# Optimization experiments

Measured on AMD Instinct MI355X. Metric: run time of the kernel, lower is better.

The kernel has to match this reference:

```python
import jax, jax.numpy as jnp
import numpy as np

N, E, F_IN, HID, HEADS = 10000, 160000, 70, 256, 4
NEG_SLOPE = 0.2


def setup_inputs() -> dict:
    key = jax.random.key(0)
    ks = jax.random.split(key, 12)
    p = lambda k, shape: jax.random.normal(k, shape, jnp.float32) * 0.05
    return dict(
        node_features=jax.random.normal(ks[0], (N, F_IN), jnp.float32),
        edge_index=jax.random.randint(ks[1], (2, E), 0, N),
        edge_attr=jax.random.normal(ks[2], (E, 4), jnp.float32),
        W1=p(ks[3], (F_IN, HEADS * HID)),
        att_src1=p(ks[4], (HEADS, HID)),
        att_dst1=p(ks[5], (HEADS, HID)),
        b1=jnp.zeros((HEADS * HID,), jnp.float32),
        W2=p(ks[6], (HEADS * HID, HID)),
        att_src2=p(ks[7], (1, HID)),
        att_dst2=p(ks[8], (1, HID)),
        b2=jnp.zeros((HID,), jnp.float32),
        Wv1=p(ks[9], (HID, 128)),
        bv1=jnp.zeros((128,), jnp.float32),
        Wv2=p(ks[10], (128, 1)),
        bv2=jnp.zeros((1,), jnp.float32),
    )


def _gat_layer(x, src, dst, W, a_src, a_dst, b, heads, ch, concat):
    """PyG GATConv (edge_dim=None, add_self_loops already applied to src/dst)."""
    n = x.shape[0]
    h = (x @ W).reshape(n, heads, ch)                      # [N,H,C]
    a_s = (h * a_src).sum(-1)                              # [N,H]
    a_d = (h * a_dst).sum(-1)                              # [N,H]
    e = jax.nn.leaky_relu(a_s[src] + a_d[dst], NEG_SLOPE)  # [E,H]
    # segment softmax over incoming edges of each destination node
    m = jax.ops.segment_max(e, dst, num_segments=n)        # [N,H]
    m = jnp.where(jnp.isfinite(m), m, 0.0)
    ex = jnp.exp(e - m[dst])
    denom = jax.ops.segment_sum(ex, dst, num_segments=n)[dst] + 1e-16
    alpha = ex / denom                                     # [E,H]
    out = jax.ops.segment_sum(h[src] * alpha[..., None], dst, num_segments=n)  # [N,H,C]
    out = out.reshape(n, heads * ch) if concat else out.mean(axis=1)
    return out + b


def reference(node_features, edge_index, edge_attr, W1, att_src1, att_dst1, b1,
              W2, att_src2, att_dst2, b2, Wv1, bv1, Wv2, bv2):
    # edge_attr is ignored: GATConv built without edge_dim has lin_edge=None.
    n = node_features.shape[0]
    loops = jnp.arange(n, dtype=edge_index.dtype)
    src = jnp.concatenate([edge_index[0], loops])
    dst = jnp.concatenate([edge_index[1], loops])
    x = jax.nn.relu(_gat_layer(node_features, src, dst, W1, att_src1, att_dst1, b1, HEADS, HID, True))
    x = jax.nn.relu(_gat_layer(x, src, dst, W2, att_src2, att_dst2, b2, 1, HID, False))
    pooled = x.mean(axis=0, keepdims=True)                 # [1,HID]
    hmid = jax.nn.gelu(pooled @ Wv1 + bv1, approximate=False)
    return hmid @ Wv2 + bv2                                # [1,1]
```

## Files before the change

kernel.cpp:

```cpp
#include <hip/hip_runtime.h>
#include <math.h>

#define NN   10000
#define NE   160000
#define NET  (NE + NN)
#define FIN  70
#define HIDC 256
#define NH   4
#define D1   1024
#define SLOPE 0.2f
#define KL1  96
#define NPB  32
#define BCAP 64

typedef float f32x4 __attribute__((ext_vector_type(4)));
typedef short bf16x8 __attribute__((ext_vector_type(8)));

__device__ __forceinline__ unsigned short f32_to_bf16(float f) {
    unsigned int u = __float_as_uint(f);
    unsigned int r = u + 0x7fffu + ((u >> 16) & 1u);
    return (unsigned short)(r >> 16);
}
__device__ __forceinline__ float bf16_to_f32(unsigned short h) {
    return __uint_as_float(((unsigned int)h) << 16);
}
__device__ __forceinline__ float leaky(float e) { return (e > 0.f) ? e : SLOPE * e; }

__device__ __forceinline__ void cp16(const unsigned short* g, unsigned short* l) {
    __builtin_amdgcn_global_load_lds((const __attribute__((address_space(1))) unsigned int*)g,
                                     (__attribute__((address_space(3))) unsigned int*)l,
                                     16, 0, 0);
}

__global__ __launch_bounds__(256) void k_prep(const float* __restrict__ W2,
                                              unsigned short* __restrict__ W2t,
                                              const float* __restrict__ W1,
                                              unsigned short* __restrict__ W1t,
                                              const float* __restrict__ asrc,
                                              const float* __restrict__ adst,
                                              float* __restrict__ was,
                                              float* __restrict__ wad,
                                              const float* __restrict__ x,
                                              unsigned short* __restrict__ xb,
                                              const int* __restrict__ ei,
                                              int* __restrict__ cnt,
                                              int* __restrict__ ssrc) {
    int b = blockIdx.x, t = threadIdx.x;
    if (b < 1024) {
        int kk = b, n = t;
        W2t[(size_t)n * 1024 + kk] = f32_to_bf16(W2[(size_t)kk * HIDC + n]);
    } else if (b < 1024 + KL1) {
        int kk = b - 1024, n = t;
#pragma unroll
        for (int h = 0; h < NH; h++) {
            float w = (kk < FIN) ? W1[(size_t)kk * D1 + h * 256 + n] : 0.f;
            W1t[((size_t)(h * 256 + n)) * KL1 + kk] = f32_to_bf16(w);
        }
    } else if (b < 1024 + KL1 + FIN) {
        int k = b - 1024 - KL1;
        __shared__ float rs[256], rd[256];
#pragma unroll
        for (int h = 0; h < NH; h++) {
            float wv = W1[(size_t)k * D1 + h * 256 + t];
            rs[t] = wv * asrc[h * 256 + t];
            rd[t] = wv * adst[h * 256 + t];
            __syncthreads();
            for (int off = 128; off > 0; off >>= 1) {
                if (t < off) { rs[t] += rs[t + off]; rd[t] += rd[t + off]; }
                __syncthreads();
            }
            if (t == 0) { was[h * FIN + k] = rs[0]; wad[h * FIN + k] = rd[0]; }
            __syncthreads();
        }
    } else if (b < 1024 + KL1 + FIN + 40) {
        int b2 = b - 1024 - KL1 - FIN;
        size_t base = (size_t)b2 * 17500;
        for (int i = t; i < 17500; i += 256)
            xb[base + i] = f32_to_bf16(x[base + i]);
    } else {
        int e = (b - 1024 - KL1 - FIN - 40) * 256 + t;
        if (e < NET) {
            int src, dst;
            if (e < NE) { src = ei[e]; dst = ei[NE + e]; }
            else        { src = e - NE; dst = src; }
            int pos = atomicAdd(&cnt[dst], 1);
            if (pos < BCAP) ssrc[dst * BCAP + pos] = src;
        }
    }
}

__global__ __launch_bounds__(256) void k_att_x(const float* __restrict__ x,
                                               const float* __restrict__ was,
                                               const float* __restrict__ wad,
                                               float* __restrict__ asn,
                                               float* __restrict__ adn) {
    __shared__ float xs[64][71];
    int t = threadIdx.x;
    int n0 = blockIdx.x * 64;
    for (int i = t; i < 64 * FIN; i += 256) {
        int r = i / FIN, k = i % FIN;
        int n = n0 + r;
        xs[r][k] = (n < NN) ? x[(size_t)n * FIN + k] : 0.f;
    }
    __syncthreads();
    if (t >= 64) return;
    int n = n0 + t;
    if (n >= NN) return;
    float a[NH] = {}, d[NH] = {};
    for (int k = 0; k < FIN; k++) {
        float xv = xs[t][k];
#pragma unroll
        for (int h = 0; h < NH; h++) {
            a[h] += xv * was[h * FIN + k];
            d[h] += xv * wad[h * FIN + k];
        }
    }
#pragma unroll
    for (int h = 0; h < NH; h++) { asn[n * NH + h] = a[h]; adn[n * NH + h] = d[h]; }
}

__global__ __launch_bounds__(64) void k_sm_aggX(const int* __restrict__ cnt,
                                                const int* __restrict__ ssrc,
                                                const float* __restrict__ as,
                                                const float* __restrict__ ad,
                                                const unsigned short* __restrict__ xb,
                                                unsigned short* __restrict__ aggXhi) {
    int d = blockIdx.x, t = threadIdx.x;
    int n = cnt[d]; if (n > BCAP) n = BCAP;
    float4 adv = *(const float4*)&ad[d * NH];
    bool v0 = t < n;
    int s0 = 0;
    float e0[NH];
    if (v0) {
        s0 = ssrc[d * BCAP + t];
        float4 a4 = *(const float4*)&as[s0 * NH];
        e0[0] = leaky(a4.x + adv.x); e0[1] = leaky(a4.y + adv.y);
        e0[2] = leaky(a4.z + adv.z); e0[3] = leaky(a4.w + adv.w);
    } else { e0[0] = e0[1] = e0[2] = e0[3] = -1e30f; }
    float m[NH] = {e0[0], e0[1], e0[2], e0[3]};
#pragma unroll
    for (int h = 0; h < NH; h++)
        for (int off = 32; off > 0; off >>= 1)
            m[h] = fmaxf(m[h], __shfl_xor(m[h], off));
    float sum[NH];
#pragma unroll
    for (int h = 0; h < NH; h++) sum[h] = v0 ? expf(e0[h] - m[h]) : 0.f;
#pragma unroll
    for (int h = 0; h < NH; h++)
        for (int off = 32; off > 0; off >>= 1)
            sum[h] += __shfl_xor(sum[h], off);
    __shared__ float al4[64][4];
    __shared__ int   sid[64];
    if (v0) {
        sid[t] = s0;
#pragma unroll
        for (int h = 0; h < NH; h++) al4[t][h] = expf(e0[h] - m[h]) / (sum[h] + 1e-16f);
    }
    __syncthreads();
    float ac[NH][2] = {};
#pragma unroll 4
    for (int j = 0; j < n; j++) {
        int s = sid[j];
        float4 al = *(const float4*)al4[j];
        float xv0 = bf16_to_f32(xb[(size_t)s * FIN + t]);
        float xv1 = (t < FIN - 64) ? bf16_to_f32(xb[(size_t)s * FIN + 64 + t]) : 0.f;
        ac[0][0] += al.x * xv0; ac[0][1] += al.x * xv1;
        ac[1][0] += al.y * xv0; ac[1][1] += al.y * xv1;
        ac[2][0] += al.z * xv0; ac[2][1] += al.z * xv1;
        ac[3][0] += al.w * xv0; ac[3][1] += al.w * xv1;
    }
#pragma unroll
    for (int h = 0; h < NH; h++) {
        size_t base = ((size_t)d * NH + h) * KL1;
        aggXhi[base + t] = f32_to_bf16(ac[h][0]);
        if (t < 32) {
            float v1 = (t < FIN - 64) ? ac[h][1] : 0.f;
            aggXhi[base + 64 + t] = f32_to_bf16(v1);
        }
    }
}

__global__ __launch_bounds__(256) void k_gemm_l1(const unsigned short* __restrict__ aggXhi,
                                                 const unsigned short* __restrict__ W1t,
                                                 const float* __restrict__ b1,
                                                 unsigned short* __restrict__ x2hi) {
    __shared__ unsigned short As[128 * 32];
    __shared__ unsigned short Bs[128 * 32];
    int t = threadIdx.x;
    int n0 = blockIdx.x * 128;
    int cb = blockIdx.y * 128;
    int h  = blockIdx.z;
    int lane = t & 63, wave = t >> 6, quad = lane >> 4, l16 = lane & 15;
    int wr = (wave & 1) * 64, wc = (wave >> 1) * 64;
    int f0 = t, f1 = t + 256;
    int ra0 = n0 + (f0 >> 2); if (ra0 >= NN) ra0 = NN - 1;
    int ra1 = n0 + (f1 >> 2); if (ra1 >= NN) ra1 = NN - 1;
    const unsigned short* ga0 = aggXhi + ((size_t)ra0 * NH + h) * KL1 + (f0 & 3) * 8;
    const unsigned short* ga1 = aggXhi + ((size_t)ra1 * NH + h) * KL1 + (f1 & 3) * 8;
    const unsigned short* gb0 = W1t + (size_t)(h * 256 + cb + (f0 >> 2)) * KL1 + (f0 & 3) * 8;
    const unsigned short* gb1 = W1t + (size_t)(h * 256 + cb + (f1 >> 2)) * KL1 + (f1 & 3) * 8;
    unsigned short* la0 = As + f0 * 8;
    unsigned short* la1 = As + f1 * 8;
    unsigned short* lb0 = Bs + f0 * 8;
    unsigned short* lb1 = Bs + f1 * 8;
    f32x4 acc[4][4] = {};
    for (int kc = 0; kc < 3; kc++) {
        cp16(ga0 + kc * 32, la0);
        cp16(ga1 + kc * 32, la1);
        cp16(gb0 + kc * 32, lb0);
        cp16(gb1 + kc * 32, lb1);
        __syncthreads();
        bf16x8 af[4], bf[4];
#pragma unroll
        for (int i = 0; i < 4; i++) af[i] = *(const bf16x8*)&As[(wr + i * 16 + l16) * 32 + quad * 8];
#pragma unroll
        for (int j = 0; j < 4; j++) bf[j] = *(const bf16x8*)&Bs[(wc + j * 16 + l16) * 32 + quad * 8];
#pragma unroll
        for (int i = 0; i < 4; i++)
#pragma unroll
            for (int j = 0; j < 4; j++)
                acc[i][j] = __builtin_amdgcn_mfma_f32_16x16x32_bf16(af[i], bf[j], acc[i][j], 0, 0, 0);
        __syncthreads();
    }
#pragma unroll
    for (int i = 0; i < 4; i++)
#pragma unroll
        for (int j = 0; j < 4; j++) {
            int colg = h * 256 + cb + wc + j * 16 + l16;
            float bb = b1[colg];
#pragma unroll
            for (int reg = 0; reg < 4; reg++) {
                int r = n0 + wr + i * 16 + quad * 4 + reg;
                if (r >= NN) continue;
                float v = fmaxf(acc[i][j][reg] + bb, 0.f);
                x2hi[(size_t)r * D1 + colg] = f32_to_bf16(v);
            }
        }
}

__global__ __launch_bounds__(256) void k_gemm2(const unsigned short* __restrict__ x2hi,
                                               const unsigned short* __restrict__ W2t,
                                               const float* __restrict__ asrc,
                                               const float* __restrict__ adst,
                                               unsigned short* __restrict__ h2bf,
                                               float* __restrict__ as2,
                                               float* __restrict__ ad2) {
    __shared__ unsigned short As[128 * 32];
    __shared__ unsigned short Bs[128 * 32];
    int t = threadIdx.x;
    int n0 = blockIdx.x * 128;
    int cb = blockIdx.y * 128;
    int lane = t & 63, wave = t >> 6, quad = lane >> 4, l16 = lane & 15;
    int wr = (wave & 1) * 64, wc = (wave >> 1) * 64;
    int f0 = t, f1 = t + 256;
    int ra0 = n0 + (f0 >> 2); if (ra0 >= NN) ra0 = NN - 1;
    int ra1 = n0 + (f1 >> 2); if (ra1 >= NN) ra1 = NN - 1;
    const unsigned short* ga0 = x2hi + (size_t)ra0 * D1 + (f0 & 3) * 8;
    const unsigned short* ga1 = x2hi + (size_t)ra1 * D1 + (f1 & 3) * 8;
    const unsigned short* gb0 = W2t + (size_t)(cb + (f0 >> 2)) * 1024 + (f0 & 3) * 8;
    const unsigned short* gb1 = W2t + (size_t)(cb + (f1 >> 2)) * 1024 + (f1 & 3) * 8;
    unsigned short* la0 = As + f0 * 8;
    unsigned short* la1 = As + f1 * 8;
    unsigned short* lb0 = Bs + f0 * 8;
    unsigned short* lb1 = Bs + f1 * 8;
    f32x4 acc[4][4] = {};
    for (int kc = 0; kc < 32; kc++) {
        cp16(ga0 + kc * 32, la0);
        cp16(ga1 + kc * 32, la1);
        cp16(gb0 + kc * 32, lb0);
        cp16(gb1 + kc * 32, lb1);
        __syncthreads();
        bf16x8 af[4], bf[4];
#pragma unroll
        for (int i = 0; i < 4; i++) af[i] = *(const bf16x8*)&As[(wr + i * 16 + l16) * 32 + quad * 8];
#pragma unroll
        for (int j = 0; j < 4; j++) bf[j] = *(const bf16x8*)&Bs[(wc + j * 16 + l16) * 32 + quad * 8];
#pragma unroll
        for (int i = 0; i < 4; i++)
#pragma unroll
            for (int j = 0; j < 4; j++)
                acc[i][j] = __builtin_amdgcn_mfma_f32_16x16x32_bf16(af[i], bf[j], acc[i][j], 0, 0, 0);
        __syncthreads();
    }
    float a2[4], d2[4];
#pragma unroll
    for (int j = 0; j < 4; j++) {
        int c = cb + wc + j * 16 + l16;
        a2[j] = asrc[c];
        d2[j] = adst[c];
    }
    float asp[4][4] = {}, adp[4][4] = {};
#pragma unroll
    for (int i = 0; i < 4; i++)
#pragma unroll
        for (int j = 0; j < 4; j++) {
            int c = cb + wc + j * 16 + l16;
#pragma unroll
            for (int reg = 0; reg < 4; reg++) {
                int r = n0 + wr + i * 16 + quad * 4 + reg;
                float v = acc[i][j][reg];
                if (r < NN) h2bf[(size_t)r * HIDC + c] = f32_to_bf16(v);
                asp[i][reg] += v * a2[j];
                adp[i][reg] += v * d2[j];
            }
        }
#pragma unroll
    for (int mask = 1; mask < 16; mask <<= 1)
#pragma unroll
        for (int i = 0; i < 4; i++)
#pragma unroll
            for (int reg = 0; reg < 4; reg++) {
                asp[i][reg] += __shfl_xor(asp[i][reg], mask);
                adp[i][reg] += __shfl_xor(adp[i][reg], mask);
            }
    if (l16 == 0) {
#pragma unroll
        for (int i = 0; i < 4; i++)
#pragma unroll
            for (int reg = 0; reg < 4; reg++) {
                int r = n0 + wr + i * 16 + quad * 4 + reg;
                if (r < NN) {
                    atomicAdd(&as2[r], asp[i][reg]);
                    atomicAdd(&ad2[r], adp[i][reg]);
                }
            }
    }
}

__global__ __launch_bounds__(256) void k_sm_aggr2(const int* __restrict__ cnt,
                                                  const int* __restrict__ ssrc,
                                                  const float* __restrict__ as,
                                                  const float* __restrict__ ad,
                                                  const unsigned short* __restrict__ h2bf,
                                                  const float* __restrict__ b,
                                                  float* __restrict__ pooled32) {
    int d = blockIdx.x, t = threadIdx.x, lane = t & 63;
    int n = cnt[d]; if (n > BCAP) n = BCAP;
    float adv = ad[d];
    bool v0 = lane < n;
    int s0 = v0 ? ssrc[d * BCAP + lane] : 0;
    float e0 = v0 ? leaky(as[s0] + adv) : -1e30f;
    float m = e0;
    for (int off = 32; off > 0; off >>= 1) m = fmaxf(m, __shfl_xor(m, off));
    float sum = v0 ? expf(e0 - m) : 0.f;
    for (int off = 32; off > 0; off >>= 1) sum += __shfl_xor(sum, off);
    float inv = 1.0f / (sum + 1e-16f);
    __shared__ float als[64];
    __shared__ int   sid[64];
    if (v0) { sid[lane] = s0; als[lane] = expf(e0 - m) * inv; }
    __syncthreads();
    float acc = 0.f;
#pragma unroll 4
    for (int j = 0; j < n; j++)
        acc += als[j] * bf16_to_f32(h2bf[(size_t)sid[j] * HIDC + t]);
    float v = fmaxf(acc + b[t], 0.f);
    atomicAdd(&pooled32[(d & (NPB - 1)) * HIDC + t], v);
}

__global__ __launch_bounds__(128) void k_mlp(const float* __restrict__ pooled32,
                                             const float* __restrict__ Wv1,
                                             const float* __restrict__ bv1,
                                             const float* __restrict__ Wv2,
                                             const float* __restrict__ bv2,
                                             float* __restrict__ out) {
    int j = threadIdx.x;
    __shared__ float ps[256];
    for (int c = j; c < HIDC; c += 128) {
        float s = 0.f;
        for (int bkt = 0; bkt < NPB; bkt++) s += pooled32[bkt * HIDC + c];
        ps[c] = s;
    }
    __syncthreads();
    float s = bv1[j];
    const float invn = 1.0f / (float)NN;
    for (int c = 0; c < HIDC; c++)
        s += (ps[c] * invn) * Wv1[c * 128 + j];
    float g = 0.5f * s * (1.0f + erff(s * 0.70710678118654752f));
    float v = g * Wv2[j];
    __shared__ float red[128];
    red[j] = v;
    __syncthreads();
    for (int off = 64; off > 0; off >>= 1) {
        if (j < off) red[j] += red[j + off];
        __syncthreads();
    }
    if (j == 0) out[0] = red[0] + bv2[0];
}

extern "C" void kernel_launch(void* const* d_in, const int* in_sizes, int n_in,
                              void* d_out, int out_size, void* d_ws, size_t ws_size,
                              hipStream_t stream) {
    const float* x_in  = (const float*)d_in[0];
    const int*   ei    = (const int*)d_in[1];
    const float* W1    = (const float*)d_in[3];
    const float* asrc1 = (const float*)d_in[4];
    const float* adst1 = (const float*)d_in[5];
    const float* b1    = (const float*)d_in[6];
    const float* W2    = (const float*)d_in[7];
    const float* asrc2 = (const float*)d_in[8];
    const float* adst2 = (const float*)d_in[9];
    const float* b2    = (const float*)d_in[10];
    const float* Wv1   = (const float*)d_in[11];
    const float* bv1   = (const float*)d_in[12];
    const float* Wv2   = (const float*)d_in[13];
    const float* bv2   = (const float*)d_in[14];
    float* out = (float*)d_out;

    char* w = (char*)d_ws;
    auto alloc = [&](size_t bytes) { char* p = w; w += (bytes + 255) & ~(size_t)255; return p; };
    unsigned short* x2hi   = (unsigned short*)alloc(2ull * NN * D1);
    unsigned short* aggXhi = (unsigned short*)alloc(2ull * NN * NH * KL1);
    unsigned short* h2bf = (unsigned short*)alloc(2ull * NN * HIDC);
    unsigned short* xb   = (unsigned short*)alloc(2ull * NN * FIN);
    unsigned short* W2t  = (unsigned short*)alloc(2ull * 256 * 1024);
    unsigned short* W1t  = (unsigned short*)alloc(2ull * NH * 256 * KL1);
    float* as1    = (float*)alloc(sizeof(float) * NN * NH);
    float* ad1    = (float*)alloc(sizeof(float) * NN * NH);
    float* was1   = (float*)alloc(sizeof(float) * NH * FIN);
    float* wad1   = (float*)alloc(sizeof(float) * NH * FIN);
    int*   ssrc   = (int*)alloc(sizeof(int) * NN * BCAP);
    char*  zbase  = alloc(NN * 4 + NPB * HIDC * 4 + NN * 4 + NN * 4);
    int*   cnt      = (int*)zbase;
    float* pooled32 = (float*)(zbase + NN * 4);
    float* as2      = (float*)(zbase + NN * 4 + NPB * HIDC * 4);
    float* ad2      = (float*)(zbase + NN * 4 + NPB * HIDC * 4 + NN * 4);

    hipMemsetAsync(zbase, 0, NN * 4 + NPB * HIDC * 4 + NN * 4 + NN * 4, stream);

    k_prep<<<1024 + KL1 + FIN + 40 + 665, 256, 0, stream>>>(
        W2, W2t, W1, W1t, asrc1, adst1, was1, wad1, x_in, xb, ei, cnt, ssrc);
    k_att_x<<<157, 256, 0, stream>>>(x_in, was1, wad1, as1, ad1);

    k_sm_aggX<<<NN, 64, 0, stream>>>(cnt, ssrc, as1, ad1, xb, aggXhi);
    {
        dim3 g((NN + 127) / 128, 2, NH);
        k_gemm_l1<<<g, 256, 0, stream>>>(aggXhi, W1t, b1, x2hi);
    }

    {
        dim3 g((NN + 127) / 128, 2);
        k_gemm2<<<g, 256, 0, stream>>>(x2hi, W2t, asrc2, adst2, h2bf, as2, ad2);
    }
    k_sm_aggr2<<<NN, 256, 0, stream>>>(cnt, ssrc, as2, ad2, h2bf, b2, pooled32);

    k_mlp<<<1, 128, 0, stream>>>(pooled32, Wv1, bv1, Wv2, bv2, out);
}
```

Measured before the change: 212.6 us.

## Fuse layer-1 attention scores into aggregation kernel and shrink gemm2 tile

Removes the separate k_att_x kernel. k_sm_aggX now stages each destination's neighbour feature rows in shared memory and computes the per-source and per-destination attention logits there from the folded weight vectors. The destination logit is read from the self-loop slot (jd_sh), and the staged rows are reused in the aggregation loop instead of being loaded from global memory again. This recomputes source logits for every edge (about 17x redundant FLOPs) to save one launch and global traffic. Separately, k_gemm2 goes from 128x128 tiles with 4 waves to 64x128 tiles with 2 waves, doubling the grid to about 314 blocks for better CU occupancy.

```diff
diff --git a/kernel.cpp b/kernel.cpp
--- a/kernel.cpp
+++ b/kernel.cpp
@@ -89,70 +89,64 @@
     }
 }
 
-__global__ __launch_bounds__(256) void k_att_x(const float* __restrict__ x,
-                                               const float* __restrict__ was,
-                                               const float* __restrict__ wad,
-                                               float* __restrict__ asn,
-                                               float* __restrict__ adn) {
-    __shared__ float xs[64][71];
-    int t = threadIdx.x;
-    int n0 = blockIdx.x * 64;
-    for (int i = t; i < 64 * FIN; i += 256) {
-        int r = i / FIN, k = i % FIN;
-        int n = n0 + r;
-        xs[r][k] = (n < NN) ? x[(size_t)n * FIN + k] : 0.f;
-    }
-    __syncthreads();
-    if (t >= 64) return;
-    int n = n0 + t;
-    if (n >= NN) return;
-    float a[NH] = {}, d[NH] = {};
-    for (int k = 0; k < FIN; k++) {
-        float xv = xs[t][k];
-#pragma unroll
-        for (int h = 0; h < NH; h++) {
-            a[h] += xv * was[h * FIN + k];
-            d[h] += xv * wad[h * FIN + k];
-        }
-    }
-#pragma unroll
-    for (int h = 0; h < NH; h++) { asn[n * NH + h] = a[h]; adn[n * NH + h] = d[h]; }
-}
-
 __global__ __launch_bounds__(64) void k_sm_aggX(const int* __restrict__ cnt,
                                                 const int* __restrict__ ssrc,
-                                                const float* __restrict__ as,
-                                                const float* __restrict__ ad,
+                                                const float* __restrict__ was,
+                                                const float* __restrict__ wad,
                                                 const unsigned short* __restrict__ xb,
                                                 unsigned short* __restrict__ aggXhi) {
     int d = blockIdx.x, t = threadIdx.x;
     int n = cnt[d]; if (n > BCAP) n = BCAP;
-    float4 adv = *(const float4*)&ad[d * NH];
+    __shared__ unsigned short xs[64][74];
+    __shared__ float wl[NH][FIN];
+    __shared__ float dl[NH][FIN];
+    __shared__ float al4[64][4];
+    __shared__ float advs[NH];
+    __shared__ int sid[64];
+    __shared__ int jd_sh;
+    for (int i = t; i < NH * FIN; i += 64) {
+        wl[i / FIN][i % FIN] = was[i];
+        dl[i / FIN][i % FIN] = wad[i];
+    }
+    if (t < n) {
+        int s0 = ssrc[d * BCAP + t];
+        sid[t] = s0;
+        if (s0 == d) jd_sh = t;
+    }
+    __syncthreads();
+    for (int j = 0; j < n; j++) {
+        int s = sid[j];
+        xs[j][t] = xb[(size_t)s * FIN + t];
+        if (t < FIN - 64) xs[j][64 + t] = xb[(size_t)s * FIN + 64 + t];
+    }
+    __syncthreads();
+    if (t < NH) {
+        int jd = jd_sh;
+        float a = 0.f;
+        for (int k = 0; k < FIN; k++) a += bf16_to_f32(xs[jd][k]) * dl[t][k];
+        advs[t] = a;
+    }
+    float a4[NH] = {};
+    if (t < n) {
+        for (int k = 0; k < FIN; k++) {
+            float xv = bf16_to_f32(xs[t][k]);
+#pragma unroll
+            for (int h = 0; h < NH; h++) a4[h] += xv * wl[h][k];
+        }
+    }
+    __syncthreads();
     bool v0 = t < n;
-    int s0 = 0;
-    float e0[NH];
+    float e0[NH], m[NH], sum[NH];
+#pragma unroll
+    for (int h = 0; h < NH; h++) e0[h] = v0 ? leaky(a4[h] + advs[h]) : -1e30f;
+#pragma unroll
+    for (int h = 0; h < NH; h++) {
+        m[h] = e0[h];
+        for (int off = 32; off > 0; off >>= 1) m[h] = fmaxf(m[h], __shfl_xor(m[h], off));
+        sum[h] = v0 ? expf(e0[h] - m[h]) : 0.f;
+        for (int off = 32; off > 0; off >>= 1) sum[h] += __shfl_xor(sum[h], off);
+    }
     if (v0) {
-        s0 = ssrc[d * BCAP + t];
-        float4 a4 = *(const float4*)&as[s0 * NH];
-        e0[0] = leaky(a4.x + adv.x); e0[1] = leaky(a4.y + adv.y);
-        e0[2] = leaky(a4.z + adv.z); e0[3] = leaky(a4.w + adv.w);
-    } else { e0[0] = e0[1] = e0[2] = e0[3] = -1e30f; }
-    float m[NH] = {e0[0], e0[1], e0[2], e0[3]};
-#pragma unroll
-    for (int h = 0; h < NH; h++)
-        for (int off = 32; off > 0; off >>= 1)
-            m[h] = fmaxf(m[h], __shfl_xor(m[h], off));
-    float sum[NH];
-#pragma unroll
-    for (int h = 0; h < NH; h++) sum[h] = v0 ? expf(e0[h] - m[h]) : 0.f;
-#pragma unroll
-    for (int h = 0; h < NH; h++)
-        for (int off = 32; off > 0; off >>= 1)
-            sum[h] += __shfl_xor(sum[h], off);
-    __shared__ float al4[64][4];
-    __shared__ int   sid[64];
-    if (v0) {
-        sid[t] = s0;
 #pragma unroll
         for (int h = 0; h < NH; h++) al4[t][h] = expf(e0[h] - m[h]) / (sum[h] + 1e-16f);
     }
@@ -160,10 +154,9 @@
     float ac[NH][2] = {};
 #pragma unroll 4
     for (int j = 0; j < n; j++) {
-        int s = sid[j];
         float4 al = *(const float4*)al4[j];
-        float xv0 = bf16_to_f32(xb[(size_t)s * FIN + t]);
-        float xv1 = (t < FIN - 64) ? bf16_to_f32(xb[(size_t)s * FIN + 64 + t]) : 0.f;
+        float xv0 = bf16_to_f32(xs[j][t]);
+        float xv1 = (t < FIN - 64) ? bf16_to_f32(xs[j][64 + t]) : 0.f;
         ac[0][0] += al.x * xv0; ac[0][1] += al.x * xv1;
         ac[1][0] += al.y * xv0; ac[1][1] += al.y * xv1;
         ac[2][0] += al.z * xv0; ac[2][1] += al.z * xv1;
@@ -238,41 +231,45 @@
         }
 }
 
-__global__ __launch_bounds__(256) void k_gemm2(const unsigned short* __restrict__ x2hi,
+__global__ __launch_bounds__(128) void k_gemm2(const unsigned short* __restrict__ x2hi,
                                                const unsigned short* __restrict__ W2t,
                                                const float* __restrict__ asrc,
                                                const float* __restrict__ adst,
                                                unsigned short* __restrict__ h2bf,
                                                float* __restrict__ as2,
                                                float* __restrict__ ad2) {
-    __shared__ unsigned short As[128 * 32];
+    __shared__ unsigned short As[64 * 32];
     __shared__ unsigned short Bs[128 * 32];
     int t = threadIdx.x;
-    int n0 = blockIdx.x * 128;
+    int n0 = blockIdx.x * 64;
     int cb = blockIdx.y * 128;
     int lane = t & 63, wave = t >> 6, quad = lane >> 4, l16 = lane & 15;
-    int wr = (wave & 1) * 64, wc = (wave >> 1) * 64;
-    int f0 = t, f1 = t + 256;
-    int ra0 = n0 + (f0 >> 2); if (ra0 >= NN) ra0 = NN - 1;
-    int ra1 = n0 + (f1 >> 2); if (ra1 >= NN) ra1 = NN - 1;
-    const unsigned short* ga0 = x2hi + (size_t)ra0 * D1 + (f0 & 3) * 8;
-    const unsigned short* ga1 = x2hi + (size_t)ra1 * D1 + (f1 & 3) * 8;
-    const unsigned short* gb0 = W2t + (size_t)(cb + (f0 >> 2)) * 1024 + (f0 & 3) * 8;
-    const unsigned short* gb1 = W2t + (size_t)(cb + (f1 >> 2)) * 1024 + (f1 & 3) * 8;
-    unsigned short* la0 = As + f0 * 8;
-    unsigned short* la1 = As + f1 * 8;
-    unsigned short* lb0 = Bs + f0 * 8;
-    unsigned short* lb1 = Bs + f1 * 8;
+    int wc = wave * 64;
+    int fa0 = t, fa1 = t + 128;
+    int raa0 = n0 + (fa0 >> 2); if (raa0 >= NN) raa0 = NN - 1;
+    int raa1 = n0 + (fa1 >> 2); if (raa1 >= NN) raa1 = NN - 1;
+    const unsigned short* ga0 = x2hi + (size_t)raa0 * D1 + (fa0 & 3) * 8;
+    const unsigned short* ga1 = x2hi + (size_t)raa1 * D1 + (fa1 & 3) * 8;
+    unsigned short* la0 = As + fa0 * 8;
+    unsigned short* la1 = As + fa1 * 8;
+    const unsigned short* gb[4];
+    unsigned short* lb[4];
+#pragma unroll
+    for (int q = 0; q < 4; q++) {
+        int f = t + q * 128;
+        gb[q] = W2t + (size_t)(cb + (f >> 2)) * 1024 + (f & 3) * 8;
+        lb[q] = Bs + f * 8;
+    }
     f32x4 acc[4][4] = {};
     for (int kc = 0; kc < 32; kc++) {
         cp16(ga0 + kc * 32, la0);
         cp16(ga1 + kc * 32, la1);
-        cp16(gb0 + kc * 32, lb0);
-        cp16(gb1 + kc * 32, lb1);
+#pragma unroll
+        for (int q = 0; q < 4; q++) cp16(gb[q] + kc * 32, lb[q]);
         __syncthreads();
         bf16x8 af[4], bf[4];
 #pragma unroll
-        for (int i = 0; i < 4; i++) af[i] = *(const bf16x8*)&As[(wr + i * 16 + l16) * 32 + quad * 8];
+        for (int i = 0; i < 4; i++) af[i] = *(const bf16x8*)&As[(i * 16 + l16) * 32 + quad * 8];
 #pragma unroll
         for (int j = 0; j < 4; j++) bf[j] = *(const bf16x8*)&Bs[(wc + j * 16 + l16) * 32 + quad * 8];
 #pragma unroll
@@ -297,7 +294,7 @@
             int c = cb + wc + j * 16 + l16;
 #pragma unroll
             for (int reg = 0; reg < 4; reg++) {
-                int r = n0 + wr + i * 16 + quad * 4 + reg;
+                int r = n0 + i * 16 + quad * 4 + reg;
                 float v = acc[i][j][reg];
                 if (r < NN) h2bf[(size_t)r * HIDC + c] = f32_to_bf16(v);
                 asp[i][reg] += v * a2[j];
@@ -318,7 +315,7 @@
         for (int i = 0; i < 4; i++)
 #pragma unroll
             for (int reg = 0; reg < 4; reg++) {
-                int r = n0 + wr + i * 16 + quad * 4 + reg;
+                int r = n0 + i * 16 + quad * 4 + reg;
                 if (r < NN) {
                     atomicAdd(&as2[r], asp[i][reg]);
                     atomicAdd(&ad2[r], adp[i][reg]);
@@ -414,8 +411,6 @@
     unsigned short* xb   = (unsigned short*)alloc(2ull * NN * FIN);
     unsigned short* W2t  = (unsigned short*)alloc(2ull * 256 * 1024);
     unsigned short* W1t  = (unsigned short*)alloc(2ull * NH * 256 * KL1);
-    float* as1    = (float*)alloc(sizeof(float) * NN * NH);
-    float* ad1    = (float*)alloc(sizeof(float) * NN * NH);
     float* was1   = (float*)alloc(sizeof(float) * NH * FIN);
     float* wad1   = (float*)alloc(sizeof(float) * NH * FIN);
     int*   ssrc   = (int*)alloc(sizeof(int) * NN * BCAP);
@@ -429,17 +424,16 @@
 
     k_prep<<<1024 + KL1 + FIN + 40 + 665, 256, 0, stream>>>(
         W2, W2t, W1, W1t, asrc1, adst1, was1, wad1, x_in, xb, ei, cnt, ssrc);
-    k_att_x<<<157, 256, 0, stream>>>(x_in, was1, wad1, as1, ad1);
-
-    k_sm_aggX<<<NN, 64, 0, stream>>>(cnt, ssrc, as1, ad1, xb, aggXhi);
+
+    k_sm_aggX<<<NN, 64, 0, stream>>>(cnt, ssrc, was1, wad1, xb, aggXhi);
     {
         dim3 g((NN + 127) / 128, 2, NH);
         k_gemm_l1<<<g, 256, 0, stream>>>(aggXhi, W1t, b1, x2hi);
     }
 
     {
-        dim3 g((NN + 127) / 128, 2);
-        k_gemm2<<<g, 256, 0, stream>>>(x2hi, W2t, asrc2, adst2, h2bf, as2, ad2);
+        dim3 g((NN + 63) / 64, 2);
+        k_gemm2<<<g, 128, 0, stream>>>(x2hi, W2t, asrc2, adst2, h2bf, as2, ad2);
     }
     k_sm_aggr2<<<NN, 256, 0, stream>>>(cnt, ssrc, as2, ad2, h2bf, b2, pooled32);
 
```

After: 235.1 us. +10.6%, slower.
